# Performance work log

Hardware: AMD Instinct MI355X
Metric: run time of the kernel (lower is better)

Reference implementation:

```python
import jax, jax.numpy as jnp
import numpy as np

GROUP = 8          # weight_group_size
QMAX = 7.0         # 2**(4-1)-1, narrow-range symmetric int4
EPS = 1e-8


def quant_dequant(w):
    """Per-group (size 8, along in_features) symmetric int4 quant-dequant.
    w: [out, in] -> dequantized [out, in]."""
    O, I = w.shape
    wg = w.reshape(O, I // GROUP, GROUP)
    scale = jnp.max(jnp.abs(wg), axis=-1, keepdims=True) / QMAX  # [O, I/G, 1]
    scale = jnp.maximum(scale, EPS)
    q = jnp.clip(jnp.round(wg / scale), -QMAX, QMAX)
    return (q * scale).reshape(O, I)


def setup_inputs() -> dict:
    key = jax.random.key(0)
    kx, kw, kb = jax.random.split(key, 3)
    tokens, din, dout = 8192, 4096, 4096
    x = jax.random.normal(kx, (tokens, din), dtype=jnp.float32)
    weight = jax.random.normal(kw, (dout, din), dtype=jnp.float32) * 0.02
    bias = jax.random.normal(kb, (dout,), dtype=jnp.float32) * 0.01
    return {"x": x, "weight": weight, "bias": bias}


def reference(x, weight, bias):
    w_deq = quant_dequant(weight)                 # [out, in]
    return jnp.dot(x, w_deq.T) + bias             # [tokens, out]
```

## Files before the change

kernel.cpp:

```cpp
#include <hip/hip_runtime.h>
#include <hip/hip_bf16.h>
#include <stdint.h>

typedef __attribute__((ext_vector_type(8))) __bf16 bf16x8;
typedef __attribute__((ext_vector_type(4))) float f32x4;
typedef __attribute__((ext_vector_type(8))) unsigned short ushort8;

typedef const void __attribute__((address_space(1))) gv_t;
typedef void __attribute__((address_space(3))) lv_t;

#define GL16(g, l) __builtin_amdgcn_global_load_lds((gv_t*)(g), (lv_t*)(l), 16, 0, 0)

__device__ __forceinline__ unsigned short f2bf(float f) {
    unsigned int u = __float_as_uint(f);
    u += 0x7fffu + ((u >> 16) & 1u);
    return (unsigned short)(u >> 16);
}

__global__ void __launch_bounds__(256) qdq_weight(const float* __restrict__ w,
                                                  unsigned short* __restrict__ wb,
                                                  int n_groups) {
    int g = blockIdx.x * 256 + threadIdx.x;
    if (g >= n_groups) return;
    const float4* p = (const float4*)w + (size_t)g * 2;
    float4 v0 = p[0], v1 = p[1];
    float t[8] = {v0.x, v0.y, v0.z, v0.w, v1.x, v1.y, v1.z, v1.w};
    float amax = 0.0f;
#pragma unroll
    for (int j = 0; j < 8; ++j) amax = fmaxf(amax, fabsf(t[j]));
    float scale = fmaxf(amax / 7.0f, 1e-8f);
    ushort8 o;
#pragma unroll
    for (int j = 0; j < 8; ++j) {
        float q = rintf(t[j] / scale);
        q = fminf(fmaxf(q, -7.0f), 7.0f);
        o[j] = f2bf(q * scale);
    }
    *((ushort8*)wb + g) = o;
}

__global__ void __launch_bounds__(256) cvt_bf16(const float* __restrict__ x,
                                                unsigned short* __restrict__ xb,
                                                int n8) {
    int i = blockIdx.x * 256 + threadIdx.x;
    if (i >= n8) return;
    const float4* p = (const float4*)x + (size_t)i * 2;
    float4 v0 = p[0], v1 = p[1];
    ushort8 o;
    o[0] = f2bf(v0.x); o[1] = f2bf(v0.y); o[2] = f2bf(v0.z); o[3] = f2bf(v0.w);
    o[4] = f2bf(v1.x); o[5] = f2bf(v1.y); o[6] = f2bf(v1.z); o[7] = f2bf(v1.w);
    *((ushort8*)xb + i) = o;
}

#define BM 256
#define BN 256
#define BK 64

#define MFMA_Q(qm, qn, AF, BF)                                                 \
    __builtin_amdgcn_s_setprio(1);                                             \
    _Pragma("unroll")                                                          \
    for (int mi = 0; mi < 4; ++mi)                                             \
        _Pragma("unroll")                                                      \
        for (int ni = 0; ni < 2; ++ni)                                         \
            _Pragma("unroll")                                                  \
            for (int ks = 0; ks < 2; ++ks)                                     \
                acc[(qm) * 4 + mi][(qn) * 2 + ni] =                            \
                    __builtin_amdgcn_mfma_f32_16x16x32_bf16(                   \
                        AF[mi][ks], BF[ni][ks],                                \
                        acc[(qm) * 4 + mi][(qn) * 2 + ni], 0, 0, 0);           \
    __builtin_amdgcn_s_setprio(0);

#define STAGE4(dst, src, kk)                                                   \
    {                                                                          \
        _Pragma("unroll")                                                      \
        for (int rr = 0; rr < 4; ++rr)                                         \
            GL16((src) + (size_t)(rr * 64 + srow) * K + (kk) + schunk,         \
                 (dst) + rr * 64 * BK + sldso);                                \
    }

__global__ void __launch_bounds__(512, 2)
gemm256(const unsigned short* __restrict__ A,
        const unsigned short* __restrict__ B,
        const float* __restrict__ bias,
        float* __restrict__ C,
        int M, int N, int K) {
    __shared__ unsigned short sA[2][BM * BK];
    __shared__ unsigned short sB[2][BN * BK];

    const int t  = threadIdx.x;
    const int w  = t >> 6;
    const int ln = t & 63;
    const int lr = ln & 15;
    const int lk = ln >> 4;
    const int wr = w >> 2;
    const int wc = w & 3;

    const int nbn = N / BN;
    const int bid = blockIdx.x;
    const int swz = ((int)gridDim.x & 7) ? bid
                  : ((bid & 7) * ((int)gridDim.x >> 3) + (bid >> 3));
    const int m0 = (swz / nbn) * BM;
    const int n0 = (swz % nbn) * BN;

    const unsigned short* gA = A + (size_t)m0 * K;
    const unsigned short* gB = B + (size_t)n0 * K;

    const int srow   = t >> 3;
    const int schunk = (((t & 7) ^ (srow & 7)) << 3);
    const int sldso  = (w * 8) * BK;

    const int sw = (lr & 7) << 3;
    const int e0 = (lk * 8) ^ sw;
    const int e1 = (32 + lk * 8) ^ sw;

    f32x4 acc[8][4];
#pragma unroll
    for (int i = 0; i < 8; ++i)
#pragma unroll
        for (int j = 0; j < 4; ++j)
            acc[i][j] = (f32x4)(0.0f);

    const int NT = K / BK;

    STAGE4(&sA[0][0], gA, 0);
    STAGE4(&sB[0][0], gB, 0);
    STAGE4(&sA[1][0], gA, BK);
    STAGE4(&sB[1][0], gB, BK);
    asm volatile("s_waitcnt vmcnt(8)" ::: "memory");
    asm volatile("s_barrier" ::: "memory");

    for (int tt = 0; tt < NT; ++tt) {
        const unsigned short* Ls_A = &sA[tt & 1][0];
        const unsigned short* Ls_B = &sB[tt & 1][0];
        unsigned short* Ld_A = &sA[tt & 1][0];
        unsigned short* Ld_B = &sB[tt & 1][0];
        const bool st = (tt + 2 < NT);
        const int k2 = (tt + 2) * BK;

        bf16x8 a0[4][2], a1[4][2], b0[2][2], b1[2][2];

#pragma unroll
        for (int mi = 0; mi < 4; ++mi) {
            const int r = (wr * 128 + mi * 16 + lr) * BK;
            a0[mi][0] = *(const bf16x8*)&Ls_A[r + e0];
            a0[mi][1] = *(const bf16x8*)&Ls_A[r + e1];
        }
#pragma unroll
        for (int ni = 0; ni < 2; ++ni) {
            const int r = (wc * 64 + ni * 16 + lr) * BK;
            b0[ni][0] = *(const bf16x8*)&Ls_B[r + e0];
            b0[ni][1] = *(const bf16x8*)&Ls_B[r + e1];
        }
        __builtin_amdgcn_s_barrier();
        MFMA_Q(0, 0, a0, b0);
        asm volatile("s_barrier" ::: "memory");

#pragma unroll
        for (int mi = 0; mi < 4; ++mi) {
            const int r = (wr * 128 + 64 + mi * 16 + lr) * BK;
            a1[mi][0] = *(const bf16x8*)&Ls_A[r + e0];
            a1[mi][1] = *(const bf16x8*)&Ls_A[r + e1];
        }
        __builtin_amdgcn_s_barrier();
        MFMA_Q(1, 0, a1, b0);
        asm volatile("s_barrier" ::: "memory");

#pragma unroll
        for (int ni = 0; ni < 2; ++ni) {
            const int r = (wc * 64 + 32 + ni * 16 + lr) * BK;
            b1[ni][0] = *(const bf16x8*)&Ls_B[r + e0];
            b1[ni][1] = *(const bf16x8*)&Ls_B[r + e1];
        }
        if (st) STAGE4(Ld_A, gA, k2);
        __builtin_amdgcn_s_barrier();
        MFMA_Q(1, 1, a1, b1);
        asm volatile("s_barrier" ::: "memory");

        if (st) STAGE4(Ld_B, gB, k2);
        __builtin_amdgcn_s_barrier();
        MFMA_Q(0, 1, a0, b1);
        if (st) asm volatile("s_waitcnt vmcnt(8)" ::: "memory");
        else    asm volatile("s_waitcnt vmcnt(0)" ::: "memory");
        asm volatile("s_barrier" ::: "memory");
    }

#pragma unroll
    for (int j = 0; j < 4; ++j) {
        const int n = n0 + wc * 64 + (j >> 1) * 32 + (j & 1) * 16 + lr;
        const float bv = bias[n];
#pragma unroll
        for (int i = 0; i < 8; ++i) {
            const int m = m0 + wr * 128 + (i >> 2) * 64 + (i & 3) * 16 + lk * 4;
            f32x4 v = acc[i][j];
            C[(size_t)(m + 0) * N + n] = v[0] + bv;
            C[(size_t)(m + 1) * N + n] = v[1] + bv;
            C[(size_t)(m + 2) * N + n] = v[2] + bv;
            C[(size_t)(m + 3) * N + n] = v[3] + bv;
        }
    }
}

extern "C" void kernel_launch(void* const* d_in, const int* in_sizes, int n_in,
                              void* d_out, int out_size, void* d_ws, size_t ws_size,
                              hipStream_t stream) {
    const float* x    = (const float*)d_in[0];
    const float* wgt  = (const float*)d_in[1];
    const float* bias = (const float*)d_in[2];
    float* out        = (float*)d_out;

    const int dout = in_sizes[2];
    const int din  = in_sizes[1] / dout;
    const int M    = in_sizes[0] / din;
    const int N    = dout, K = din;

    unsigned short* xb = (unsigned short*)d_ws;
    unsigned short* wb = xb + (size_t)M * K;

    const int ng_w = (N * K) / 8;
    qdq_weight<<<(ng_w + 255) / 256, 256, 0, stream>>>(wgt, wb, ng_w);

    const int n8_x = (M * K) / 8;
    cvt_bf16<<<(n8_x + 255) / 256, 256, 0, stream>>>(x, xb, n8_x);

    const int nwg = (M / BM) * (N / BN);
    gemm256<<<nwg, 512, 0, stream>>>(xb, wb, bias, out, M, N, K);
}
```

Measured before the change: 311.4 us.

## Split LDS tiles into halves and stage each half as soon as consumed

The shared tiles are split into two 128-row halves per operand, and the main loop is unrolled by two k-steps. Each half is refilled from global memory right after the last wave reads it, rather than refilling whole tiles late in the iteration. This spreads the global-to-LDS loads more evenly across the MFMA phases to improve overlap. It also remaps which rows each wave reads from A and B. The cost is more complex indexing and tighter vmcnt accounting.

```diff
diff --git a/kernel.cpp b/kernel.cpp
--- a/kernel.cpp
+++ b/kernel.cpp
@@ -70,13 +70,39 @@
                         acc[(qm) * 4 + mi][(qn) * 2 + ni], 0, 0, 0);           \
     __builtin_amdgcn_s_setprio(0);
 
-#define STAGE4(dst, src, kk)                                                   \
+#define STAGE_A(b, h, kk)                                                      \
     {                                                                          \
-        _Pragma("unroll")                                                      \
-        for (int rr = 0; rr < 4; ++rr)                                         \
-            GL16((src) + (size_t)(rr * 64 + srow) * K + (kk) + schunk,         \
-                 (dst) + rr * 64 * BK + sldso);                                \
-    }
+        GL16(gA + (size_t)((h) * 64 + srow) * K + (kk) + schunk,               \
+             &sA[b][h][0] + sldso);                                            \
+        GL16(gA + (size_t)((h) * 64 + 128 + srow) * K + (kk) + schunk,         \
+             &sA[b][h][64 * BK] + sldso);                                      \
+    }
+#define STAGE_B(b, h, kk)                                                      \
+    {                                                                          \
+        GL16(gB + (size_t)((h) * 32 + brow) * K + (kk) + schunk,               \
+             &sB[b][h][0] + sldso);                                            \
+        GL16(gB + (size_t)((h) * 32 + 128 + brow) * K + (kk) + schunk,         \
+             &sB[b][h][64 * BK] + sldso);                                      \
+    }
+
+#define READ_A(dst, b, h)                                                      \
+    _Pragma("unroll")                                                          \
+    for (int mi = 0; mi < 4; ++mi) {                                           \
+        const int s_ = (wr * 64 + mi * 16 + lr) * BK;                          \
+        dst[mi][0] = *(const bf16x8*)&sA[b][h][s_ + e0];                       \
+        dst[mi][1] = *(const bf16x8*)&sA[b][h][s_ + e1];                       \
+    }
+#define READ_B(dst, b, h)                                                      \
+    _Pragma("unroll")                                                          \
+    for (int ni = 0; ni < 2; ++ni) {                                           \
+        const int s_ = (bcol + ni * 16 + lr) * BK;                             \
+        dst[ni][0] = *(const bf16x8*)&sB[b][h][s_ + e0];                       \
+        dst[ni][1] = *(const bf16x8*)&sB[b][h][s_ + e1];                       \
+    }
+
+#define OPEN_BAR()  __builtin_amdgcn_s_barrier()
+#define CLOSE_BAR() asm volatile("s_barrier" ::: "memory")
+#define VM(n)       asm volatile("s_waitcnt vmcnt(" #n ")" ::: "memory")
 
 __global__ void __launch_bounds__(512, 2)
 gemm256(const unsigned short* __restrict__ A,
@@ -84,8 +110,8 @@
         const float* __restrict__ bias,
         float* __restrict__ C,
         int M, int N, int K) {
-    __shared__ unsigned short sA[2][BM * BK];
-    __shared__ unsigned short sB[2][BN * BK];
+    __shared__ unsigned short sA[2][2][128 * BK];
+    __shared__ unsigned short sB[2][2][128 * BK];
 
     const int t  = threadIdx.x;
     const int w  = t >> 6;
@@ -94,6 +120,7 @@
     const int lk = ln >> 4;
     const int wr = w >> 2;
     const int wc = w & 3;
+    const int bcol = (wc >> 1) * 64 + (wc & 1) * 32;
 
     const int nbn = N / BN;
     const int bid = blockIdx.x;
@@ -106,6 +133,7 @@
     const unsigned short* gB = B + (size_t)n0 * K;
 
     const int srow   = t >> 3;
+    const int brow   = (srow & 31) + ((srow >> 5) << 6);
     const int schunk = (((t & 7) ^ (srow & 7)) << 3);
     const int sldso  = (w * 8) * BK;
 
@@ -122,66 +150,68 @@
 
     const int NT = K / BK;
 
-    STAGE4(&sA[0][0], gA, 0);
-    STAGE4(&sB[0][0], gB, 0);
-    STAGE4(&sA[1][0], gA, BK);
-    STAGE4(&sB[1][0], gB, BK);
-    asm volatile("s_waitcnt vmcnt(8)" ::: "memory");
-    asm volatile("s_barrier" ::: "memory");
-
-    for (int tt = 0; tt < NT; ++tt) {
-        const unsigned short* Ls_A = &sA[tt & 1][0];
-        const unsigned short* Ls_B = &sB[tt & 1][0];
-        unsigned short* Ld_A = &sA[tt & 1][0];
-        unsigned short* Ld_B = &sB[tt & 1][0];
-        const bool st = (tt + 2 < NT);
-        const int k2 = (tt + 2) * BK;
+    STAGE_A(0, 0, 0); STAGE_B(0, 0, 0);
+    STAGE_A(0, 1, 0); STAGE_B(0, 1, 0);
+    STAGE_A(1, 0, BK); STAGE_B(1, 0, BK);
+    VM(4);
+    CLOSE_BAR();
+
+    for (int it = 0; it < NT / 2; ++it) {
+        const int t0  = 2 * it;
+        const int kC  = (t0 + 1) * BK;
+        const int kN0 = (t0 + 2) * BK;
+        const int kN1 = (t0 + 3) * BK;
+        const bool st = (t0 + 2 < NT);
 
         bf16x8 a0[4][2], a1[4][2], b0[2][2], b1[2][2];
 
-#pragma unroll
-        for (int mi = 0; mi < 4; ++mi) {
-            const int r = (wr * 128 + mi * 16 + lr) * BK;
-            a0[mi][0] = *(const bf16x8*)&Ls_A[r + e0];
-            a0[mi][1] = *(const bf16x8*)&Ls_A[r + e1];
-        }
-#pragma unroll
-        for (int ni = 0; ni < 2; ++ni) {
-            const int r = (wc * 64 + ni * 16 + lr) * BK;
-            b0[ni][0] = *(const bf16x8*)&Ls_B[r + e0];
-            b0[ni][1] = *(const bf16x8*)&Ls_B[r + e1];
-        }
-        __builtin_amdgcn_s_barrier();
+        READ_A(a0, 0, 0); READ_B(b0, 0, 0);
+        STAGE_A(1, 1, kC);
+        OPEN_BAR();
         MFMA_Q(0, 0, a0, b0);
-        asm volatile("s_barrier" ::: "memory");
-
-#pragma unroll
-        for (int mi = 0; mi < 4; ++mi) {
-            const int r = (wr * 128 + 64 + mi * 16 + lr) * BK;
-            a1[mi][0] = *(const bf16x8*)&Ls_A[r + e0];
-            a1[mi][1] = *(const bf16x8*)&Ls_A[r + e1];
-        }
-        __builtin_amdgcn_s_barrier();
+        CLOSE_BAR();
+
+        READ_A(a1, 0, 1);
+        STAGE_B(1, 1, kC);
+        OPEN_BAR();
         MFMA_Q(1, 0, a1, b0);
-        asm volatile("s_barrier" ::: "memory");
-
-#pragma unroll
-        for (int ni = 0; ni < 2; ++ni) {
-            const int r = (wc * 64 + 32 + ni * 16 + lr) * BK;
-            b1[ni][0] = *(const bf16x8*)&Ls_B[r + e0];
-            b1[ni][1] = *(const bf16x8*)&Ls_B[r + e1];
-        }
-        if (st) STAGE4(Ld_A, gA, k2);
-        __builtin_amdgcn_s_barrier();
+        CLOSE_BAR();
+
+        READ_B(b1, 0, 1);
+        if (st) STAGE_A(0, 0, kN0);
+        OPEN_BAR();
         MFMA_Q(1, 1, a1, b1);
-        asm volatile("s_barrier" ::: "memory");
-
-        if (st) STAGE4(Ld_B, gB, k2);
-        __builtin_amdgcn_s_barrier();
+        CLOSE_BAR();
+
+        if (st) STAGE_B(0, 0, kN0);
+        OPEN_BAR();
         MFMA_Q(0, 1, a0, b1);
-        if (st) asm volatile("s_waitcnt vmcnt(8)" ::: "memory");
-        else    asm volatile("s_waitcnt vmcnt(0)" ::: "memory");
-        asm volatile("s_barrier" ::: "memory");
+        if (st) VM(4); else VM(0);
+        CLOSE_BAR();
+
+        READ_A(a0, 1, 0); READ_B(b0, 1, 0);
+        if (st) STAGE_A(0, 1, kN0);
+        OPEN_BAR();
+        MFMA_Q(0, 0, a0, b0);
+        CLOSE_BAR();
+
+        READ_A(a1, 1, 1);
+        if (st) STAGE_B(0, 1, kN0);
+        OPEN_BAR();
+        MFMA_Q(1, 0, a1, b0);
+        CLOSE_BAR();
+
+        READ_B(b1, 1, 1);
+        if (st) STAGE_A(1, 0, kN1);
+        OPEN_BAR();
+        MFMA_Q(1, 1, a1, b1);
+        CLOSE_BAR();
+
+        if (st) STAGE_B(1, 0, kN1);
+        OPEN_BAR();
+        MFMA_Q(0, 1, a0, b1);
+        if (st) VM(4); else VM(0);
+        CLOSE_BAR();
     }
 
 #pragma unroll
```

New measurement: 306.8 us. About the same (-1.5%).

## Restructure GEMM to 128x256 tiles with BK=32 and 4-wave phased pipeline

Applied to the files above, without the earlier changes.

Replaces the 256x256x64 tile, 8-wave GEMM with a 128x256x32 tile run by 4 waves. Each wave owns a 128x64 output slab and reads all of A plus its own B columns. The main loop is rewritten as a two-buffer ping-pong, unrolled by two, with explicit barriers, lgkmcnt waits and sched_barriers around the MFMA phases. The intent is to cut LDS footprint and raise occupancy while overlapping global-to-LDS staging with MFMA work. The cost is less data reuse per tile and more synchronisation per K step, and the full vmcnt(0) waits may stall the loads.

```diff
diff --git a/kernel.cpp b/kernel.cpp
--- a/kernel.cpp
+++ b/kernel.cpp
@@ -52,34 +52,53 @@
     *((ushort8*)xb + i) = o;
 }
 
-#define BM 256
+#define BM 128
 #define BN 256
-#define BK 64
-
-#define MFMA_Q(qm, qn, AF, BF)                                                 \
+#define BK 32
+
+#define MFMA_PH(q)                                                             \
     __builtin_amdgcn_s_setprio(1);                                             \
     _Pragma("unroll")                                                          \
-    for (int mi = 0; mi < 4; ++mi)                                             \
+    for (int mi = 0; mi < 8; ++mi)                                             \
         _Pragma("unroll")                                                      \
-        for (int ni = 0; ni < 2; ++ni)                                         \
-            _Pragma("unroll")                                                  \
-            for (int ks = 0; ks < 2; ++ks)                                     \
-                acc[(qm) * 4 + mi][(qn) * 2 + ni] =                            \
-                    __builtin_amdgcn_mfma_f32_16x16x32_bf16(                   \
-                        AF[mi][ks], BF[ni][ks],                                \
-                        acc[(qm) * 4 + mi][(qn) * 2 + ni], 0, 0, 0);           \
+        for (int nn = 0; nn < 2; ++nn)                                         \
+            acc[mi][(q) * 2 + nn] =                                            \
+                __builtin_amdgcn_mfma_f32_16x16x32_bf16(                       \
+                    af[mi], bf[(q) * 2 + nn], acc[mi][(q) * 2 + nn], 0, 0, 0); \
     __builtin_amdgcn_s_setprio(0);
 
-#define STAGE4(dst, src, kk)                                                   \
+#define STAGE_A(b, kk)                                                         \
     {                                                                          \
         _Pragma("unroll")                                                      \
-        for (int rr = 0; rr < 4; ++rr)                                         \
-            GL16((src) + (size_t)(rr * 64 + srow) * K + (kk) + schunk,         \
-                 (dst) + rr * 64 * BK + sldso);                                \
-    }
-
-__global__ void __launch_bounds__(512, 2)
-gemm256(const unsigned short* __restrict__ A,
+        for (int j = 0; j < 2; ++j)                                            \
+            GL16(gA + (size_t)(j * 64 + srow4) * K + (kk) + schunk2,           \
+                 &sA[b][(j * 64 + w * 16) * BK]);                              \
+    }
+#define STAGE_B2(b, kk, j0)                                                    \
+    {                                                                          \
+        _Pragma("unroll")                                                      \
+        for (int j = (j0); j < (j0) + 2; ++j)                                  \
+            GL16(gB + (size_t)(j * 64 + srow4) * K + (kk) + schunk2,           \
+                 &sB[b][(j * 64 + w * 16) * BK]);                              \
+    }
+
+#define READ_A(b)                                                              \
+    _Pragma("unroll")                                                          \
+    for (int mi = 0; mi < 8; ++mi)                                             \
+        af[mi] = *(const bf16x8*)&sA[b][(mi * 16 + lr) * BK + ce];
+#define READ_B2(b, q)                                                          \
+    _Pragma("unroll")                                                          \
+    for (int nn = 0; nn < 2; ++nn)                                             \
+        bf[(q) * 2 + nn] =                                                     \
+            *(const bf16x8*)&sB[b][(bcol + ((q) * 2 + nn) * 16 + lr) * BK + ce];
+
+#define BAR_()     asm volatile("s_barrier" ::: "memory")
+#define VM0_()     asm volatile("s_waitcnt vmcnt(0)" ::: "memory")
+#define LGKM0_()   asm volatile("s_waitcnt lgkmcnt(0)" ::: "memory")
+#define SCHEDBAR() __builtin_amdgcn_sched_barrier(0)
+
+__global__ void __launch_bounds__(256, 2)
+gemm128(const unsigned short* __restrict__ A,
         const unsigned short* __restrict__ B,
         const float* __restrict__ bias,
         float* __restrict__ C,
@@ -92,8 +111,7 @@
     const int ln = t & 63;
     const int lr = ln & 15;
     const int lk = ln >> 4;
-    const int wr = w >> 2;
-    const int wc = w & 3;
+    const int bcol = w * 64;
 
     const int nbn = N / BN;
     const int bid = blockIdx.x;
@@ -105,13 +123,10 @@
     const unsigned short* gA = A + (size_t)m0 * K;
     const unsigned short* gB = B + (size_t)n0 * K;
 
-    const int srow   = t >> 3;
-    const int schunk = (((t & 7) ^ (srow & 7)) << 3);
-    const int sldso  = (w * 8) * BK;
-
-    const int sw = (lr & 7) << 3;
-    const int e0 = (lk * 8) ^ sw;
-    const int e1 = (32 + lk * 8) ^ sw;
+    const int srow4   = w * 16 + (ln >> 2);
+    const int schunk2 = (((ln & 3) ^ ((ln >> 3) & 3)) << 3);
+
+    const int ce = ((lk ^ ((lr >> 1) & 3)) << 3);
 
     f32x4 acc[8][4];
 #pragma unroll
@@ -120,77 +135,55 @@
         for (int j = 0; j < 4; ++j)
             acc[i][j] = (f32x4)(0.0f);
 
+    bf16x8 af[8], bf[4];
+
     const int NT = K / BK;
 
-    STAGE4(&sA[0][0], gA, 0);
-    STAGE4(&sB[0][0], gB, 0);
-    STAGE4(&sA[1][0], gA, BK);
-    STAGE4(&sB[1][0], gB, BK);
-    asm volatile("s_waitcnt vmcnt(8)" ::: "memory");
-    asm volatile("s_barrier" ::: "memory");
-
-    for (int tt = 0; tt < NT; ++tt) {
-        const unsigned short* Ls_A = &sA[tt & 1][0];
-        const unsigned short* Ls_B = &sB[tt & 1][0];
-        unsigned short* Ld_A = &sA[tt & 1][0];
-        unsigned short* Ld_B = &sB[tt & 1][0];
-        const bool st = (tt + 2 < NT);
-        const int k2 = (tt + 2) * BK;
-
-        bf16x8 a0[4][2], a1[4][2], b0[2][2], b1[2][2];
-
-#pragma unroll
-        for (int mi = 0; mi < 4; ++mi) {
-            const int r = (wr * 128 + mi * 16 + lr) * BK;
-            a0[mi][0] = *(const bf16x8*)&Ls_A[r + e0];
-            a0[mi][1] = *(const bf16x8*)&Ls_A[r + e1];
-        }
-#pragma unroll
-        for (int ni = 0; ni < 2; ++ni) {
-            const int r = (wc * 64 + ni * 16 + lr) * BK;
-            b0[ni][0] = *(const bf16x8*)&Ls_B[r + e0];
-            b0[ni][1] = *(const bf16x8*)&Ls_B[r + e1];
-        }
-        __builtin_amdgcn_s_barrier();
-        MFMA_Q(0, 0, a0, b0);
-        asm volatile("s_barrier" ::: "memory");
-
-#pragma unroll
-        for (int mi = 0; mi < 4; ++mi) {
-            const int r = (wr * 128 + 64 + mi * 16 + lr) * BK;
-            a1[mi][0] = *(const bf16x8*)&Ls_A[r + e0];
-            a1[mi][1] = *(const bf16x8*)&Ls_A[r + e1];
-        }
-        __builtin_amdgcn_s_barrier();
-        MFMA_Q(1, 0, a1, b0);
-        asm volatile("s_barrier" ::: "memory");
-
-#pragma unroll
-        for (int ni = 0; ni < 2; ++ni) {
-            const int r = (wc * 64 + 32 + ni * 16 + lr) * BK;
-            b1[ni][0] = *(const bf16x8*)&Ls_B[r + e0];
-            b1[ni][1] = *(const bf16x8*)&Ls_B[r + e1];
-        }
-        if (st) STAGE4(Ld_A, gA, k2);
-        __builtin_amdgcn_s_barrier();
-        MFMA_Q(1, 1, a1, b1);
-        asm volatile("s_barrier" ::: "memory");
-
-        if (st) STAGE4(Ld_B, gB, k2);
-        __builtin_amdgcn_s_barrier();
-        MFMA_Q(0, 1, a0, b1);
-        if (st) asm volatile("s_waitcnt vmcnt(8)" ::: "memory");
-        else    asm volatile("s_waitcnt vmcnt(0)" ::: "memory");
-        asm volatile("s_barrier" ::: "memory");
+    STAGE_A(0, 0);
+    STAGE_B2(0, 0, 0);
+    STAGE_B2(0, 0, 2);
+    VM0_();
+    BAR_();
+
+    for (int it = 0; it < NT / 2; ++it) {
+        const int t0  = 2 * it;
+        const int kn1 = (t0 + 1) * BK;
+        const int kn2 = (t0 + 2) * BK;
+        const bool st2 = (t0 + 2 < NT);
+
+        READ_A(0); READ_B2(0, 0);
+        STAGE_A(1, kn1); STAGE_B2(1, kn1, 0);
+        BAR_(); LGKM0_(); SCHEDBAR();
+        MFMA_PH(0);
+        BAR_();
+        READ_B2(0, 1);
+        STAGE_B2(1, kn1, 2);
+        BAR_(); LGKM0_(); SCHEDBAR();
+        MFMA_PH(1);
+        VM0_();
+        BAR_();
+
+        READ_A(1); READ_B2(1, 0);
+        if (st2) { STAGE_A(0, kn2); STAGE_B2(0, kn2, 0); }
+        BAR_(); LGKM0_(); SCHEDBAR();
+        MFMA_PH(0);
+        BAR_();
+
+        READ_B2(1, 1);
+        if (st2) STAGE_B2(0, kn2, 2);
+        BAR_(); LGKM0_(); SCHEDBAR();
+        MFMA_PH(1);
+        VM0_();
+        BAR_();
     }
 
 #pragma unroll
     for (int j = 0; j < 4; ++j) {
-        const int n = n0 + wc * 64 + (j >> 1) * 32 + (j & 1) * 16 + lr;
+        const int n = n0 + bcol + j * 16 + lr;
         const float bv = bias[n];
 #pragma unroll
         for (int i = 0; i < 8; ++i) {
-            const int m = m0 + wr * 128 + (i >> 2) * 64 + (i & 3) * 16 + lk * 4;
+            const int m = m0 + i * 16 + lk * 4;
             f32x4 v = acc[i][j];
             C[(size_t)(m + 0) * N + n] = v[0] + bv;
             C[(size_t)(m + 1) * N + n] = v[1] + bv;
@@ -223,5 +216,5 @@
     cvt_bf16<<<(n8_x + 255) / 256, 256, 0, stream>>>(x, xb, n8_x);
 
     const int nwg = (M / BM) * (N / BN);
-    gemm256<<<nwg, 512, 0, stream>>>(xb, wb, bias, out, M, N, K);
-}
+    gemm128<<<nwg, 256, 0, stream>>>(xb, wb, bias, out, M, N, K);
+}
```

Result: slower. 329.2 us (+5.7%).

## Switch GEMM to 4-wave 128x128 per-wave tiles with simple double buffering

Applied to the files above, without the earlier changes.

Replaces the 8-wave, 2-block-per-CU GEMM, with its four-phase barrier-interleaved schedule, by a 4-wave kernel. Each wave computes a 128x128 subtile (8x8 MFMA accumulators), and the loop prefetches the next K tile, computes, then waits on vmcnt(0) and a barrier. More reuse per wave cuts LDS read traffic per MFMA. In exchange it holds 256 accumulator registers per lane, drops to one block per CU, and loses the fine-grained overlap between load waits and MFMA phases.

```diff
diff --git a/kernel.cpp b/kernel.cpp
--- a/kernel.cpp
+++ b/kernel.cpp
@@ -56,34 +56,23 @@
 #define BN 256
 #define BK 64
 
-#define MFMA_Q(qm, qn, AF, BF)                                                 \
-    __builtin_amdgcn_s_setprio(1);                                             \
-    _Pragma("unroll")                                                          \
-    for (int mi = 0; mi < 4; ++mi)                                             \
-        _Pragma("unroll")                                                      \
-        for (int ni = 0; ni < 2; ++ni)                                         \
-            _Pragma("unroll")                                                  \
-            for (int ks = 0; ks < 2; ++ks)                                     \
-                acc[(qm) * 4 + mi][(qn) * 2 + ni] =                            \
-                    __builtin_amdgcn_mfma_f32_16x16x32_bf16(                   \
-                        AF[mi][ks], BF[ni][ks],                                \
-                        acc[(qm) * 4 + mi][(qn) * 2 + ni], 0, 0, 0);           \
-    __builtin_amdgcn_s_setprio(0);
+#define BAR_()   asm volatile("s_barrier" ::: "memory")
+#define VM0_()   asm volatile("s_waitcnt vmcnt(0)" ::: "memory")
 
-#define STAGE4(dst, src, kk)                                                   \
+#define STAGE_T(sdst, gsrc, b, kk)                                             \
     {                                                                          \
         _Pragma("unroll")                                                      \
-        for (int rr = 0; rr < 4; ++rr)                                         \
-            GL16((src) + (size_t)(rr * 64 + srow) * K + (kk) + schunk,         \
-                 (dst) + rr * 64 * BK + sldso);                                \
+        for (int rr = 0; rr < 8; ++rr)                                         \
+            GL16(gsrc + (size_t)(rr * 32 + srow) * K + (kk) + schunk,          \
+                 &sdst[b][(rr * 32 + w * 8) * BK]);                            \
     }
 
-__global__ void __launch_bounds__(512, 2)
-gemm256(const unsigned short* __restrict__ A,
-        const unsigned short* __restrict__ B,
-        const float* __restrict__ bias,
-        float* __restrict__ C,
-        int M, int N, int K) {
+__global__ void __launch_bounds__(256, 1)
+gemmBW(const unsigned short* __restrict__ A,
+       const unsigned short* __restrict__ B,
+       const float* __restrict__ bias,
+       float* __restrict__ C,
+       int M, int N, int K) {
     __shared__ unsigned short sA[2][BM * BK];
     __shared__ unsigned short sB[2][BN * BK];
 
@@ -92,8 +81,8 @@
     const int ln = t & 63;
     const int lr = ln & 15;
     const int lk = ln >> 4;
-    const int wr = w >> 2;
-    const int wc = w & 3;
+    const int wr = w >> 1;
+    const int wc = w & 1;
 
     const int nbn = N / BN;
     const int bid = blockIdx.x;
@@ -107,91 +96,69 @@
 
     const int srow   = t >> 3;
     const int schunk = (((t & 7) ^ (srow & 7)) << 3);
-    const int sldso  = (w * 8) * BK;
 
     const int sw = (lr & 7) << 3;
     const int e0 = (lk * 8) ^ sw;
     const int e1 = (32 + lk * 8) ^ sw;
 
-    f32x4 acc[8][4];
+    f32x4 acc[8][8];
 #pragma unroll
     for (int i = 0; i < 8; ++i)
 #pragma unroll
-        for (int j = 0; j < 4; ++j)
+        for (int j = 0; j < 8; ++j)
             acc[i][j] = (f32x4)(0.0f);
 
     const int NT = K / BK;
 
-    STAGE4(&sA[0][0], gA, 0);
-    STAGE4(&sB[0][0], gB, 0);
-    STAGE4(&sA[1][0], gA, BK);
-    STAGE4(&sB[1][0], gB, BK);
-    asm volatile("s_waitcnt vmcnt(8)" ::: "memory");
-    asm volatile("s_barrier" ::: "memory");
+    STAGE_T(sA, gA, 0, 0);
+    STAGE_T(sB, gB, 0, 0);
+    VM0_();
+    BAR_();
 
     for (int tt = 0; tt < NT; ++tt) {
-        const unsigned short* Ls_A = &sA[tt & 1][0];
-        const unsigned short* Ls_B = &sB[tt & 1][0];
-        unsigned short* Ld_A = &sA[tt & 1][0];
-        unsigned short* Ld_B = &sB[tt & 1][0];
-        const bool st = (tt + 2 < NT);
-        const int k2 = (tt + 2) * BK;
+        const int cur = tt & 1;
+        const int nxt = cur ^ 1;
 
-        bf16x8 a0[4][2], a1[4][2], b0[2][2], b1[2][2];
+        if (tt + 1 < NT) {
+            const int kk = (tt + 1) * BK;
+            STAGE_T(sA, gA, nxt, kk);
+            STAGE_T(sB, gB, nxt, kk);
+        }
+
+        bf16x8 af[8][2];
+#pragma unroll
+        for (int mi = 0; mi < 8; ++mi) {
+            const int s_ = (wr * 128 + mi * 16 + lr) * BK;
+            af[mi][0] = *(const bf16x8*)&sA[cur][s_ + e0];
+            af[mi][1] = *(const bf16x8*)&sA[cur][s_ + e1];
+        }
 
 #pragma unroll
-        for (int mi = 0; mi < 4; ++mi) {
-            const int r = (wr * 128 + mi * 16 + lr) * BK;
-            a0[mi][0] = *(const bf16x8*)&Ls_A[r + e0];
-            a0[mi][1] = *(const bf16x8*)&Ls_A[r + e1];
+        for (int ni = 0; ni < 8; ++ni) {
+            const int s_ = (wc * 128 + ni * 16 + lr) * BK;
+            bf16x8 b0 = *(const bf16x8*)&sB[cur][s_ + e0];
+            bf16x8 b1 = *(const bf16x8*)&sB[cur][s_ + e1];
+#pragma unroll
+            for (int mi = 0; mi < 8; ++mi) {
+                acc[mi][ni] = __builtin_amdgcn_mfma_f32_16x16x32_bf16(
+                    af[mi][0], b0, acc[mi][ni], 0, 0, 0);
+                acc[mi][ni] = __builtin_amdgcn_mfma_f32_16x16x32_bf16(
+                    af[mi][1], b1, acc[mi][ni], 0, 0, 0);
+            }
         }
-#pragma unroll
-        for (int ni = 0; ni < 2; ++ni) {
-            const int r = (wc * 64 + ni * 16 + lr) * BK;
-            b0[ni][0] = *(const bf16x8*)&Ls_B[r + e0];
-            b0[ni][1] = *(const bf16x8*)&Ls_B[r + e1];
-        }
-        __builtin_amdgcn_s_barrier();
-        MFMA_Q(0, 0, a0, b0);
-        asm volatile("s_barrier" ::: "memory");
 
-#pragma unroll
-        for (int mi = 0; mi < 4; ++mi) {
-            const int r = (wr * 128 + 64 + mi * 16 + lr) * BK;
-            a1[mi][0] = *(const bf16x8*)&Ls_A[r + e0];
-            a1[mi][1] = *(const bf16x8*)&Ls_A[r + e1];
-        }
-        __builtin_amdgcn_s_barrier();
-        MFMA_Q(1, 0, a1, b0);
-        asm volatile("s_barrier" ::: "memory");
-
-#pragma unroll
-        for (int ni = 0; ni < 2; ++ni) {
-            const int r = (wc * 64 + 32 + ni * 16 + lr) * BK;
-            b1[ni][0] = *(const bf16x8*)&Ls_B[r + e0];
-            b1[ni][1] = *(const bf16x8*)&Ls_B[r + e1];
-        }
-        if (st) STAGE4(Ld_A, gA, k2);
-        __builtin_amdgcn_s_barrier();
-        MFMA_Q(1, 1, a1, b1);
-        asm volatile("s_barrier" ::: "memory");
-
-        if (st) STAGE4(Ld_B, gB, k2);
-        __builtin_amdgcn_s_barrier();
-        MFMA_Q(0, 1, a0, b1);
-        if (st) asm volatile("s_waitcnt vmcnt(8)" ::: "memory");
-        else    asm volatile("s_waitcnt vmcnt(0)" ::: "memory");
-        asm volatile("s_barrier" ::: "memory");
+        VM0_();
+        BAR_();
     }
 
 #pragma unroll
-    for (int j = 0; j < 4; ++j) {
-        const int n = n0 + wc * 64 + (j >> 1) * 32 + (j & 1) * 16 + lr;
+    for (int ni = 0; ni < 8; ++ni) {
+        const int n = n0 + wc * 128 + ni * 16 + lr;
         const float bv = bias[n];
 #pragma unroll
-        for (int i = 0; i < 8; ++i) {
-            const int m = m0 + wr * 128 + (i >> 2) * 64 + (i & 3) * 16 + lk * 4;
-            f32x4 v = acc[i][j];
+        for (int mi = 0; mi < 8; ++mi) {
+            const int m = m0 + wr * 128 + mi * 16 + lk * 4;
+            f32x4 v = acc[mi][ni];
             C[(size_t)(m + 0) * N + n] = v[0] + bv;
             C[(size_t)(m + 1) * N + n] = v[1] + bv;
             C[(size_t)(m + 2) * N + n] = v[2] + bv;
@@ -223,5 +190,5 @@
     cvt_bf16<<<(n8_x + 255) / 256, 256, 0, stream>>>(x, xb, n8_x);
 
     const int nwg = (M / BM) * (N / BN);
-    gemm256<<<nwg, 512, 0, stream>>>(xb, wb, bias, out, M, N, K);
+    gemmBW<<<nwg, 256, 0, stream>>>(xb, wb, bias, out, M, N, K);
 }
```

Result: slower. 352.7 us (+13.2%).
